# Kernel optimization log

Measured on AMD Instinct MI355X. Metric: run time of the kernel, lower is better.

The kernel has to match this reference:

```python
import jax, jax.numpy as jnp
import numpy as np

DIM = 1024
HEADS = 16
DIM_HEAD = 64
INNER = HEADS * DIM_HEAD  # 1024
EPS = 1e-5


def layer_norm(x, gamma, beta):
    mu = jnp.mean(x, axis=-1, keepdims=True)
    var = jnp.var(x, axis=-1, keepdims=True)
    return (x - mu) * jax.lax.rsqrt(var + EPS) * gamma + beta


def setup_inputs() -> dict:
    key = jax.random.key(0)
    ks = jax.random.split(key, 8)
    b, n, ctx = 2, 2048, 2048
    x = jax.random.normal(ks[0], (b, n, DIM), dtype=jnp.float32)
    context = jax.random.normal(ks[1], (b, ctx, DIM), dtype=jnp.float32)
    context_mask = jnp.ones((b, ctx), dtype=bool)
    # params (torch Linear weights, stored as [in, out] for x @ W)
    g1 = jnp.ones((DIM,), jnp.float32); b1 = jnp.zeros((DIM,), jnp.float32)
    g2 = jnp.ones((DIM,), jnp.float32); b2 = jnp.zeros((DIM,), jnp.float32)
    s = 1.0 / np.sqrt(DIM)
    Wq = jax.random.normal(ks[2], (DIM, INNER), jnp.float32) * s
    Wkv = jax.random.normal(ks[3], (DIM, 2 * INNER), jnp.float32) * s
    Wo = jax.random.normal(ks[4], (INNER, DIM), jnp.float32) * (1.0 / np.sqrt(INNER))
    bo = jnp.zeros((DIM,), jnp.float32)
    return dict(x=x, context=context, context_mask=context_mask,
                g1=g1, b1=b1, g2=g2, b2=b2, Wq=Wq, Wkv=Wkv, Wo=Wo, bo=bo)


def reference(x, context, context_mask, g1, b1, g2, b2, Wq, Wkv, Wo, bo):
    scale = DIM_HEAD ** -0.5
    xn = layer_norm(x, g1, b1)
    cn = layer_norm(context, g2, b2)
    q = xn @ Wq                                  # [b, i, inner]
    kv_x = xn @ Wkv
    kv_c = cn @ Wkv
    k_in, v_in = jnp.split(kv_x, 2, axis=-1)
    k_c, v_c = jnp.split(kv_c, 2, axis=-1)
    k = jnp.concatenate([k_c, k_in], axis=1)     # [b, j, inner]
    v = jnp.concatenate([v_c, v_in], axis=1)

    def split_heads(t):
        b_, n_, _ = t.shape
        return t.reshape(b_, n_, HEADS, DIM_HEAD).transpose(0, 2, 1, 3)

    q, k, v = map(split_heads, (q, k, v))        # [b, h, n, d]
    q = q * scale
    i, j = q.shape[2], k.shape[2]
    mask_value = -jnp.finfo(q.dtype).max

    sim = jnp.einsum('bhid,bhjd->bhij', q, k)
    # context mask padded with True over the self (input) keys
    cm = jnp.pad(context_mask, ((0, 0), (0, j - context_mask.shape[-1])), constant_values=True)
    sim = jnp.where(cm[:, None, None, :], sim, mask_value)
    # causal mask: key position (shifted) strictly after query position
    causal = jnp.triu(jnp.ones((i, j), dtype=bool), k=j - i + 1)
    sim = jnp.where(causal[None, None], mask_value, sim)

    attn = jax.nn.softmax(sim, axis=-1)
    out = jnp.einsum('bhij,bhjd->bhid', attn, v)
    out = out.transpose(0, 2, 1, 3).reshape(x.shape[0], i, INNER)
    return out @ Wo + bo
```

## Files before the change

kernel.cpp:

```cpp
#include <hip/hip_runtime.h>
#include <hip/hip_bf16.h>

#define BB 2
#define NQ 2048
#define NCTX 2048
#define DIMM 1024
#define NH 16
#define DH 64
#define NKV 4096
#define LOG2E 1.44269504088896340736f

typedef float f32x4  __attribute__((ext_vector_type(4)));
typedef float f32x16 __attribute__((ext_vector_type(16)));
typedef short s16x8  __attribute__((ext_vector_type(8)));
typedef unsigned u32x4 __attribute__((ext_vector_type(4)));

__device__ __forceinline__ unsigned short f2bf(float f){
  __hip_bfloat16 h = __float2bfloat16(f);
  return *reinterpret_cast<unsigned short*>(&h);
}

__device__ __forceinline__ unsigned pk2(float a, float b){
  unsigned r;
  asm("v_cvt_pk_bf16_f32 %0, %1, %2" : "=v"(r) : "v"(a), "v"(b));
  return r;
}

__device__ __forceinline__ void cp16(const void* g, void* l){
  __builtin_amdgcn_global_load_lds(
    (const __attribute__((address_space(1))) unsigned int*)(unsigned long long)g,
    (__attribute__((address_space(3))) unsigned int*)(unsigned int)(unsigned long long)l,
    16, 0, 0);
}

__device__ __forceinline__ f32x16 zero16(){
  f32x16 z;
  #pragma unroll
  for (int i=0;i<16;i++) z[i]=0.f;
  return z;
}

__global__ __launch_bounds__(256) void ln2_kernel(const float* __restrict__ x,
    const float* __restrict__ ctx,
    const float* __restrict__ g1, const float* __restrict__ b1,
    const float* __restrict__ g2, const float* __restrict__ b2,
    unsigned short* __restrict__ xn, unsigned short* __restrict__ cn){
  int row = blockIdx.x;
  const float *src, *g, *bta; unsigned short* dst; int r;
  if (row < BB*NQ){ src = x;   g = g1; bta = b1; dst = xn; r = row; }
  else            { src = ctx; g = g2; bta = b2; dst = cn; r = row - BB*NQ; }
  int t = threadIdx.x;
  const float4* xr = (const float4*)(src + (size_t)r*DIMM);
  float4 v = xr[t];
  float s  = v.x+v.y+v.z+v.w;
  float sq = v.x*v.x+v.y*v.y+v.z*v.z+v.w*v.w;
  #pragma unroll
  for (int off=32; off>0; off>>=1){ s += __shfl_down(s, off); sq += __shfl_down(sq, off); }
  __shared__ float red[8];
  int w = t>>6;
  if ((t&63)==0){ red[w]=s; red[w+4]=sq; }
  __syncthreads();
  s  = red[0]+red[1]+red[2]+red[3];
  sq = red[4]+red[5]+red[6]+red[7];
  float mean = s*(1.0f/DIMM);
  float var  = sq*(1.0f/DIMM) - mean*mean;
  float rstd = rsqrtf(var + 1e-5f);
  float4 gv = ((const float4*)g)[t];
  float4 bv = ((const float4*)bta)[t];
  unsigned int o0 = f2bf((v.x-mean)*rstd*gv.x + bv.x);
  unsigned int o1 = f2bf((v.y-mean)*rstd*gv.y + bv.y);
  unsigned int o2 = f2bf((v.z-mean)*rstd*gv.z + bv.z);
  unsigned int o3 = f2bf((v.w-mean)*rstd*gv.w + bv.w);
  uint2 pk; pk.x = o0 | (o1<<16); pk.y = o2 | (o3<<16);
  ((uint2*)(dst + (size_t)r*DIMM))[t] = pk;
}

__global__ __launch_bounds__(256) void wconv3_kernel(const float* __restrict__ Wq,
    const float* __restrict__ Wkv, const float* __restrict__ Wo,
    unsigned short* __restrict__ wpk, unsigned short* __restrict__ woT){
  __shared__ float tile[32][33];
  int bx = blockIdx.x;
  const float* src; unsigned short* dst; int N; float scale; int nb;
  if (bx < 32)      { src=Wq;  dst=wpk;                      N=1024; scale=0.125f; nb=bx; }
  else if (bx < 96) { src=Wkv; dst=wpk + (size_t)1024*1024;  N=2048; scale=1.0f;   nb=bx-32; }
  else              { src=Wo;  dst=woT;                      N=1024; scale=1.0f;   nb=bx-96; }
  int n0 = nb*32, k0 = blockIdx.y*32;
  int c = threadIdx.x & 31, r0 = threadIdx.x >> 5;
  #pragma unroll
  for (int i=0;i<4;i++){
    int r = r0 + i*8;
    tile[r][c] = src[(size_t)(k0+r)*N + n0 + c];
  }
  __syncthreads();
  #pragma unroll
  for (int i=0;i<4;i++){
    int r = r0 + i*8;
    dst[(size_t)(n0+r)*1024 + k0 + c] = f2bf(tile[c][r]*scale);
  }
}

#define BM 128
#define BN 128
#define BK 64
template<int MODE>
__global__ __launch_bounds__(256) void gemm_kernel(
    const unsigned short* __restrict__ A,
    const unsigned short* __restrict__ BT,
    unsigned short* __restrict__ D0,
    unsigned short* __restrict__ D1,
    unsigned short* __restrict__ D2,
    float* __restrict__ FO,
    const float* __restrict__ bias,
    int K){
  __shared__ unsigned short As[BM*BK];
  __shared__ unsigned short Bs[BN*BK];
  int t = threadIdx.x;
  int w = t>>6, l = t&63, lr = l&15, lg = l>>4;
  int wm = w>>1, wn = w&1;
  const unsigned short* Ab = A  + (size_t)(blockIdx.y*BM)*K;
  const unsigned short* Bb = BT + (size_t)(blockIdx.x*BN)*K;
  f32x4 acc[4][4];
  #pragma unroll
  for (int i=0;i<4;i++)
    #pragma unroll
    for (int j=0;j<4;j++) acc[i][j] = (f32x4){0.f,0.f,0.f,0.f};
  int nk = K >> 6;
  for (int kt=0; kt<nk; ++kt){
    __syncthreads();
    #pragma unroll
    for (int q=0;q<4;q++){
      int row = w*32 + q*8 + (l>>3);
      size_t go = (size_t)row*K + kt*64 + (l&7)*8;
      cp16(Ab + go, &As[(w*32+q*8)*64]);
      cp16(Bb + go, &Bs[(w*32+q*8)*64]);
    }
    __syncthreads();
    #pragma unroll
    for (int kk=0;kk<2;kk++){
      s16x8 af[4], bfr[4];
      #pragma unroll
      for (int mf=0;mf<4;mf++) af[mf]  = *(const s16x8*)&As[(wm*64+mf*16+lr)*64 + kk*32 + lg*8];
      #pragma unroll
      for (int nf=0;nf<4;nf++) bfr[nf] = *(const s16x8*)&Bs[(wn*64+nf*16+lr)*64 + kk*32 + lg*8];
      #pragma unroll
      for (int mf=0;mf<4;mf++)
        #pragma unroll
        for (int nf=0;nf<4;nf++)
          acc[mf][nf] = __builtin_amdgcn_mfma_f32_16x16x32_bf16(af[mf], bfr[nf], acc[mf][nf], 0,0,0);
    }
  }
  int rbase = blockIdx.y*BM + wm*64;
  int cbase = blockIdx.x*BN + wn*64;
  #pragma unroll
  for (int mf=0;mf<4;mf++){
    #pragma unroll
    for (int nf=0;nf<4;nf++){
      #pragma unroll
      for (int rr=0;rr<4;rr++){
        int r = rbase + mf*16 + lg*4 + rr;
        int c = cbase + nf*16 + lr;
        float val = acc[mf][nf][rr];
        if (MODE == 2){
          FO[(size_t)r*1024 + c] = val + bias[c];
        } else if (MODE == 0){
          int b = r >> 11, rl = r & 2047;
          unsigned short bv = f2bf(val);
          if (c < 1024)      D0[((size_t)b*NQ + rl)*1024 + c] = bv;
          else if (c < 2048) D1[((size_t)b*NKV + NCTX + rl)*1024 + (c-1024)] = bv;
          else               D2[((size_t)b*NKV + NCTX + rl)*1024 + (c-2048)] = bv;
        } else {
          int b = r >> 11, rl = r & 2047;
          unsigned short bv = f2bf(val);
          if (c < 1024) D0[((size_t)b*NKV + rl)*1024 + c] = bv;
          else          D1[((size_t)b*NKV + rl)*1024 + (c-1024)] = bv;
        }
      }
    }
  }
}

__global__ __launch_bounds__(256) void vtrans_kernel(const unsigned short* __restrict__ V,
    unsigned short* __restrict__ VT){
  __shared__ unsigned short tl[64][72];
  int j0 = blockIdx.x*64, h = blockIdx.y, b = blockIdx.z;
  int tid = threadIdx.x;
  int r = tid>>3, c8 = (tid&7)*8;
  const unsigned short* src = V + ((size_t)(b*NKV + j0))*1024 + h*64;
  #pragma unroll
  for (int p=0;p<2;p++){
    int row = r + p*32;
    *(s16x8*)&tl[row][c8] = *(const s16x8*)(src + (size_t)row*1024 + c8);
  }
  __syncthreads();
  unsigned short* dst = VT + ((size_t)(b*16+h)*64)*4096 + j0;
  #pragma unroll
  for (int p=0;p<2;p++){
    int d = r + p*32;
    s16x8 o;
    #pragma unroll
    for (int e=0;e<8;e++) o[e] = (short)tl[c8+e][d];
    *(s16x8*)(dst + (size_t)d*4096 + c8) = o;
  }
}

__global__ __launch_bounds__(256) void attn_kernel(
    const unsigned short* __restrict__ Q,
    const unsigned short* __restrict__ Kg,
    const unsigned short* __restrict__ VT,
    unsigned short* __restrict__ O){
  __shared__ unsigned short Ks[64*64];
  __shared__ unsigned short Vs[64*64];
  int bx = blockIdx.x;
  int qb = 15 - (bx >> 5);
  int hb = bx & 31;
  int h = hb & 15, b = hb >> 4;
  int i0 = qb*128;
  int tid = threadIdx.x;
  int w = tid>>6, l = tid&63;
  int q5 = l&31, hi = l>>5;

  int row0 = tid>>3, sl = tid&7;
  const unsigned short* Kb = Kg + (size_t)b*NKV*1024 + h*64;
  const unsigned short* Vb = VT + ((size_t)(b*16+h)*64)*4096;
  size_t kg0 = (size_t)row0*1024 + sl*8;
  size_t kg1 = kg0 + (size_t)32*1024;
  size_t vg0 = (size_t)row0*4096 + sl*8;
  size_t vg1 = vg0 + (size_t)32*4096;
  int sw0 = row0*128      + ((sl*16) ^ ((row0&7)<<4));
  int sw1 = (row0+32)*128 + ((sl*16) ^ ((row0&7)<<4));

  const unsigned short* Qr = Q + ((size_t)(b*NQ + i0 + w*32 + q5))*1024 + h*64 + hi*8;
  s16x8 qf[4];
  #pragma unroll
  for (int t=0;t<4;t++) qf[t] = *(const s16x8*)(Qr + t*16);

  f32x16 o0 = zero16(), o1 = zero16();
  float mref = -1e30f, m2 = 0.f, lsum = 0.f;

  int nkb = (NCTX + i0 + 128) >> 6;
  s16x8 kr0 = *(const s16x8*)(Kb + kg0);
  s16x8 kr1 = *(const s16x8*)(Kb + kg1);
  s16x8 vr0 = *(const s16x8*)(Vb + vg0);
  s16x8 vr1 = *(const s16x8*)(Vb + vg1);

  for (int kb=0; kb<nkb; ++kb){
    int j0 = kb*64;
    __syncthreads();
    *(s16x8*)((char*)Ks + sw0) = kr0;
    *(s16x8*)((char*)Ks + sw1) = kr1;
    *(s16x8*)((char*)Vs + sw0) = vr0;
    *(s16x8*)((char*)Vs + sw1) = vr1;
    if (kb+1 < nkb){
      size_t ko = (size_t)(kb+1)*64*1024;
      int vo = (kb+1)*64;
      kr0 = *(const s16x8*)(Kb + ko + kg0);
      kr1 = *(const s16x8*)(Kb + ko + kg1);
      vr0 = *(const s16x8*)(Vb + vo + vg0);
      vr1 = *(const s16x8*)(Vb + vo + vg1);
    }
    __syncthreads();

    f32x16 s0 = zero16(), s1 = zero16();
    __builtin_amdgcn_s_setprio(1);
    #pragma unroll
    for (int t=0;t<4;t++){
      int xo = (t*32 + hi*16) ^ ((q5&7)<<4);
      s16x8 kf0 = *(const s16x8*)((char*)Ks + q5*128 + xo);
      s16x8 kf1 = *(const s16x8*)((char*)Ks + (q5+32)*128 + xo);
      s0 = __builtin_amdgcn_mfma_f32_32x32x16_bf16(kf0, qf[t], s0, 0,0,0);
      s1 = __builtin_amdgcn_mfma_f32_32x32x16_bf16(kf1, qf[t], s1, 0,0,0);
    }
    __builtin_amdgcn_s_setprio(0);

    if (j0 + 63 > NCTX + i0 + w*32){
      int iq = i0 + w*32 + q5;
      #pragma unroll
      for (int r=0;r<16;r++){
        int j = j0 + ((r&3)+8*(r>>2)+4*hi);
        if (j      > NCTX + iq) s0[r] = -1e30f;
        if (j + 32 > NCTX + iq) s1[r] = -1e30f;
      }
    }

    float t0=-1e30f, t1=-1e30f, t2=-1e30f, t3=-1e30f;
    #pragma unroll
    for (int r=0;r<16;r+=4){
      t0 = fmaxf(t0, fmaxf(s0[r  ], s1[r  ]));
      t1 = fmaxf(t1, fmaxf(s0[r+1], s1[r+1]));
      t2 = fmaxf(t2, fmaxf(s0[r+2], s1[r+2]));
      t3 = fmaxf(t3, fmaxf(s0[r+3], s1[r+3]));
    }
    float pm = fmaxf(fmaxf(t0,t1), fmaxf(t2,t3));
    pm = fmaxf(pm, __shfl_xor(pm, 32));
    if (__any(pm - mref > 8.0f)){
      float mnew = fmaxf(mref, pm);
      float alpha = exp2f((mref - mnew)*LOG2E);
      mref = mnew; m2 = mnew*LOG2E;
      lsum *= alpha;
      int ai = __builtin_bit_cast(int, alpha);
      #pragma unroll
      for (int r=0;r<16;r++){
        int cr = (r&3)+8*(r>>2)+4*hi;
        float av = __builtin_bit_cast(float, __builtin_amdgcn_ds_bpermute(cr<<2, ai));
        o0[r] *= av; o1[r] *= av;
      }
    }
    float e0=0.f, e1=0.f, e2=0.f, e3=0.f;
    #pragma unroll
    for (int r=0;r<16;r+=4){
      float a0 = exp2f(fmaf(s0[r  ], LOG2E, -m2));
      float a1 = exp2f(fmaf(s0[r+1], LOG2E, -m2));
      float a2 = exp2f(fmaf(s0[r+2], LOG2E, -m2));
      float a3 = exp2f(fmaf(s0[r+3], LOG2E, -m2));
      float b0 = exp2f(fmaf(s1[r  ], LOG2E, -m2));
      float b1 = exp2f(fmaf(s1[r+1], LOG2E, -m2));
      float b2 = exp2f(fmaf(s1[r+2], LOG2E, -m2));
      float b3 = exp2f(fmaf(s1[r+3], LOG2E, -m2));
      s0[r]=a0; s0[r+1]=a1; s0[r+2]=a2; s0[r+3]=a3;
      s1[r]=b0; s1[r+1]=b1; s1[r+2]=b2; s1[r+3]=b3;
      e0 += a0 + b0; e1 += a1 + b1; e2 += a2 + b2; e3 += a3 + b3;
    }
    float ps = (e0+e1) + (e2+e3);
    ps += __shfl_xor(ps, 32);
    lsum += ps;

    s16x8 pa[4];
    #pragma unroll
    for (int t=0;t<4;t++){
      const f32x16& pp = (t<2) ? s0 : s1;
      int B8 = (t&1)*8;
      unsigned u0 = pk2(pp[B8+0], pp[B8+1]);
      unsigned u1 = pk2(pp[B8+2], pp[B8+3]);
      unsigned v0 = pk2(pp[B8+4], pp[B8+5]);
      unsigned v1 = pk2(pp[B8+6], pp[B8+7]);
      asm("v_permlane32_swap_b32 %0, %1" : "+v"(u0), "+v"(v0));
      asm("v_permlane32_swap_b32 %0, %1" : "+v"(u1), "+v"(v1));
      pa[t] = __builtin_bit_cast(s16x8, (u32x4){u0, u1, v0, v1});
    }

    __builtin_amdgcn_s_setprio(1);
    #pragma unroll
    for (int t=0;t<4;t++){
      int xo = (t*32 + hi*16) ^ ((q5&7)<<4);
      s16x8 vb0 = *(const s16x8*)((char*)Vs + q5*128 + xo);
      s16x8 vb1 = *(const s16x8*)((char*)Vs + (q5+32)*128 + xo);
      o0 = __builtin_amdgcn_mfma_f32_32x32x16_bf16(pa[t], vb0, o0, 0,0,0);
      o1 = __builtin_amdgcn_mfma_f32_32x32x16_bf16(pa[t], vb1, o1, 0,0,0);
    }
    __builtin_amdgcn_s_setprio(0);
  }

  float inv = 1.0f/lsum;
  int ii = __builtin_bit_cast(int, inv);
  #pragma unroll
  for (int r=0;r<16;r++){
    int cr = (r&3)+8*(r>>2)+4*hi;
    float sc = __builtin_bit_cast(float, __builtin_amdgcn_ds_bpermute(cr<<2, ii));
    int qg = i0 + w*32 + cr;
    unsigned short* op = O + ((size_t)(b*NQ + qg))*1024 + h*64 + q5;
    op[0]  = f2bf(o0[r]*sc);
    op[32] = f2bf(o1[r]*sc);
  }
}

extern "C" void kernel_launch(void* const* d_in, const int* in_sizes, int n_in,
                              void* d_out, int out_size, void* d_ws, size_t ws_size,
                              hipStream_t stream){
  const float* x   = (const float*)d_in[0];
  const float* ctx = (const float*)d_in[1];
  const float* g1  = (const float*)d_in[3];
  const float* b1  = (const float*)d_in[4];
  const float* g2  = (const float*)d_in[5];
  const float* b2  = (const float*)d_in[6];
  const float* Wq  = (const float*)d_in[7];
  const float* Wkv = (const float*)d_in[8];
  const float* Wo  = (const float*)d_in[9];
  const float* bo  = (const float*)d_in[10];
  float* out = (float*)d_out;

  unsigned short* xn  = (unsigned short*)d_ws;
  unsigned short* cn  = xn  + (size_t)BB*NQ*DIMM;
  unsigned short* qbf = cn  + (size_t)BB*NCTX*DIMM;
  unsigned short* kbf = qbf + (size_t)BB*NQ*1024;
  unsigned short* vbf = kbf + (size_t)BB*NKV*1024;
  unsigned short* oa  = vbf + (size_t)BB*NKV*1024;
  unsigned short* wpk = oa  + (size_t)BB*NQ*1024;
  unsigned short* woT = wpk + (size_t)3072*1024;
  unsigned short* vT  = xn;

  wconv3_kernel<<<dim3(128,32),256,0,stream>>>(Wq, Wkv, Wo, wpk, woT);
  ln2_kernel<<<dim3(BB*(NQ+NCTX)),256,0,stream>>>(x, ctx, g1, b1, g2, b2, xn, cn);
  gemm_kernel<0><<<dim3(3072/BN,(BB*NQ)/BM),256,0,stream>>>(
      xn, wpk, qbf, kbf, vbf, nullptr, nullptr, 1024);
  gemm_kernel<1><<<dim3(2048/BN,(BB*NCTX)/BM),256,0,stream>>>(
      cn, wpk + (size_t)1024*1024, kbf, vbf, nullptr, nullptr, nullptr, 1024);
  vtrans_kernel<<<dim3(64,16,2),256,0,stream>>>(vbf, vT);
  attn_kernel<<<dim3(512),256,0,stream>>>(qbf, kbf, vT, oa);
  gemm_kernel<2><<<dim3(1024/BN,(BB*NQ)/BM),256,0,stream>>>(
      oa, woT, nullptr, nullptr, nullptr, out, bo, 1024);
}
```

Baseline: 343.5 us.

## Merge QKV and context KV GEMMs into one pipelined 256x256 tile kernel

Replaces the two separate projection GEMM launches with one 320-block kernel using 256x256 tiles, 512 threads and 8 waves. The kernel streams K slices into LDS through a multi-buffered async copy pipeline with explicit vmcnt waits, barriers and setprio around the MFMA bursts. The aim is more data reuse per tile, memory latency hidden behind compute, and one fewer launch. In exchange it uses 128KB of LDS, limiting occupancy to one block per CU, and only 320 blocks exist to cover the GPU.

```diff
diff --git a/kernel.cpp b/kernel.cpp
--- a/kernel.cpp
+++ b/kernel.cpp
@@ -99,16 +99,132 @@
   }
 }
 
+__global__ __launch_bounds__(512) void qkv8_kernel(
+    const unsigned short* __restrict__ Xn,
+    const unsigned short* __restrict__ Cn,
+    const unsigned short* __restrict__ Wpk,
+    unsigned short* __restrict__ Qb,
+    unsigned short* __restrict__ Kb2,
+    unsigned short* __restrict__ Vb2){
+  __shared__ __align__(16) unsigned short As[4][128*64];
+  __shared__ __align__(16) unsigned short Bsh[4][128*64];
+  int bx = blockIdx.x;
+  const unsigned short *Abase, *Bbase; int mt, nt, isctx;
+  if (bx < 192){ Abase = Xn; Bbase = Wpk; mt = bx/12; nt = bx%12; isctx = 0; }
+  else { int b2 = bx-192; Abase = Cn; Bbase = Wpk + (size_t)1024*1024; mt = b2/8; nt = b2%8; isctx = 1; }
+  const char* Ab = (const char*)(Abase + (size_t)mt*256*1024);
+  const char* Bb = (const char*)(Bbase + (size_t)nt*256*1024);
+  int tid = threadIdx.x; int w = tid>>6, l = tid&63;
+  int wm = w>>2, wn = w&3, lr15 = l&15, lg = l>>4;
+  f32x4 acc[8][4];
+  #pragma unroll
+  for (int i=0;i<8;i++)
+    #pragma unroll
+    for (int j=0;j<4;j++) acc[i][j] = (f32x4){0.f,0.f,0.f,0.f};
+
+#define STAGEA(kt,h,par) do{ \
+  char* _l = (char*)As + ((par)*2+(h))*16384; \
+  _Pragma("unroll") for (int _q=0;_q<2;_q++){ \
+    int _c = tid + _q*512; int _lr = _c>>3; int _kb = (_c&7)*16; \
+    int _gr = ((_lr>>6)*128) + (h)*64 + (_lr&63); \
+    cp16(Ab + (size_t)_gr*2048 + (size_t)(kt)*128 + _kb, _l + _c*16); \
+  } }while(0)
+#define STAGEB(kt,h,par) do{ \
+  char* _l = (char*)Bsh + ((par)*2+(h))*16384; \
+  _Pragma("unroll") for (int _q=0;_q<2;_q++){ \
+    int _c = tid + _q*512; int _lr = _c>>3; int _kb = (_c&7)*16; \
+    int _gr = ((_lr>>5)*64) + (h)*32 + (_lr&31); \
+    cp16(Bb + (size_t)_gr*2048 + (size_t)(kt)*128 + _kb, _l + _c*16); \
+  } }while(0)
+#define VM4 asm volatile("s_waitcnt vmcnt(4)" ::: "memory")
+#define VM0 asm volatile("s_waitcnt vmcnt(0)" ::: "memory")
+#define NOST ((void)0)
+#define PHASE(mh,nh,par,STG,WAITV) do{ \
+  s16x8 _af[4][2], _bf[2][2]; \
+  const char* _pa = (const char*)As + ((par)*2+(mh))*16384; \
+  const char* _pb = (const char*)Bsh + ((par)*2+(nh))*16384; \
+  _Pragma("unroll") for (int _j=0;_j<4;_j++) \
+    _Pragma("unroll") for (int _kk=0;_kk<2;_kk++) \
+      _af[_j][_kk] = *(const s16x8*)(_pa + (wm*64 + _j*16 + lr15)*128 + _kk*64 + lg*16); \
+  _Pragma("unroll") for (int _jn=0;_jn<2;_jn++) \
+    _Pragma("unroll") for (int _kk=0;_kk<2;_kk++) \
+      _bf[_jn][_kk] = *(const s16x8*)(_pb + (wn*32 + _jn*16 + lr15)*128 + _kk*64 + lg*16); \
+  STG; \
+  WAITV; \
+  __builtin_amdgcn_s_barrier(); \
+  asm volatile("s_waitcnt lgkmcnt(0)" ::: "memory"); \
+  __builtin_amdgcn_sched_barrier(0); \
+  __builtin_amdgcn_s_setprio(1); \
+  _Pragma("unroll") for (int _j=0;_j<4;_j++) \
+    _Pragma("unroll") for (int _jn=0;_jn<2;_jn++){ \
+      acc[(mh)*4+_j][(nh)*2+_jn] = __builtin_amdgcn_mfma_f32_16x16x32_bf16(_af[_j][0], _bf[_jn][0], acc[(mh)*4+_j][(nh)*2+_jn], 0,0,0); \
+      acc[(mh)*4+_j][(nh)*2+_jn] = __builtin_amdgcn_mfma_f32_16x16x32_bf16(_af[_j][1], _bf[_jn][1], acc[(mh)*4+_j][(nh)*2+_jn], 0,0,0); \
+    } \
+  __builtin_amdgcn_s_setprio(0); \
+  __builtin_amdgcn_s_barrier(); }while(0)
+
+  STAGEA(0,0,0); STAGEB(0,0,0); STAGEA(0,1,0); STAGEB(0,1,0);
+  STAGEA(1,0,1); STAGEB(1,0,1);
+  VM4;
+  __builtin_amdgcn_s_barrier();
+
+  for (int i=0;i<7;i++){
+    int c = 2*i;
+    PHASE(0,0,0, STAGEA(c+1,1,1), NOST);
+    PHASE(0,1,0, STAGEB(c+1,1,1), NOST);
+    PHASE(1,0,0, STAGEA(c+2,0,0), NOST);
+    PHASE(1,1,0, STAGEB(c+2,0,0), VM4);
+    PHASE(0,0,1, STAGEA(c+2,1,0), NOST);
+    PHASE(0,1,1, STAGEB(c+2,1,0), NOST);
+    PHASE(1,0,1, STAGEA(c+3,0,1), NOST);
+    PHASE(1,1,1, STAGEB(c+3,0,1), VM4);
+  }
+  PHASE(0,0,0, STAGEA(15,1,1), NOST);
+  PHASE(0,1,0, STAGEB(15,1,1), NOST);
+  PHASE(1,0,0, NOST, NOST);
+  PHASE(1,1,0, NOST, VM0);
+  PHASE(0,0,1, NOST, NOST);
+  PHASE(0,1,1, NOST, NOST);
+  PHASE(1,0,1, NOST, NOST);
+  PHASE(1,1,1, NOST, NOST);
+
+  int nblk = nt>>2;
+  int coff = (nt&3)*256 + wn*64;
+  #pragma unroll
+  for (int fq=0; fq<8; fq++){
+    #pragma unroll
+    for (int fn=0; fn<4; fn++){
+      #pragma unroll
+      for (int rr=0; rr<4; rr++){
+        int r = mt*256 + wm*128 + fq*16 + lg*4 + rr;
+        int cc = coff + fn*16 + lr15;
+        int b = r>>11, rl = r&2047;
+        unsigned short bv = f2bf(acc[fq][fn][rr]);
+        if (!isctx){
+          if (nblk==0)      Qb [((size_t)b*NQ  + rl)*1024 + cc] = bv;
+          else if (nblk==1) Kb2[((size_t)b*NKV + NCTX + rl)*1024 + cc] = bv;
+          else              Vb2[((size_t)b*NKV + NCTX + rl)*1024 + cc] = bv;
+        } else {
+          if (nblk==0)      Kb2[((size_t)b*NKV + rl)*1024 + cc] = bv;
+          else              Vb2[((size_t)b*NKV + rl)*1024 + cc] = bv;
+        }
+      }
+    }
+  }
+#undef STAGEA
+#undef STAGEB
+#undef VM4
+#undef VM0
+#undef NOST
+#undef PHASE
+}
+
 #define BM 128
 #define BN 128
 #define BK 64
-template<int MODE>
-__global__ __launch_bounds__(256) void gemm_kernel(
+__global__ __launch_bounds__(256) void gemm2_kernel(
     const unsigned short* __restrict__ A,
     const unsigned short* __restrict__ BT,
-    unsigned short* __restrict__ D0,
-    unsigned short* __restrict__ D1,
-    unsigned short* __restrict__ D2,
     float* __restrict__ FO,
     const float* __restrict__ bias,
     int K){
@@ -159,21 +275,7 @@
       for (int rr=0;rr<4;rr++){
         int r = rbase + mf*16 + lg*4 + rr;
         int c = cbase + nf*16 + lr;
-        float val = acc[mf][nf][rr];
-        if (MODE == 2){
-          FO[(size_t)r*1024 + c] = val + bias[c];
-        } else if (MODE == 0){
-          int b = r >> 11, rl = r & 2047;
-          unsigned short bv = f2bf(val);
-          if (c < 1024)      D0[((size_t)b*NQ + rl)*1024 + c] = bv;
-          else if (c < 2048) D1[((size_t)b*NKV + NCTX + rl)*1024 + (c-1024)] = bv;
-          else               D2[((size_t)b*NKV + NCTX + rl)*1024 + (c-2048)] = bv;
-        } else {
-          int b = r >> 11, rl = r & 2047;
-          unsigned short bv = f2bf(val);
-          if (c < 1024) D0[((size_t)b*NKV + rl)*1024 + c] = bv;
-          else          D1[((size_t)b*NKV + rl)*1024 + (c-1024)] = bv;
-        }
+        FO[(size_t)r*1024 + c] = acc[mf][nf][rr] + bias[c];
       }
     }
   }
@@ -390,12 +492,9 @@
 
   wconv3_kernel<<<dim3(128,32),256,0,stream>>>(Wq, Wkv, Wo, wpk, woT);
   ln2_kernel<<<dim3(BB*(NQ+NCTX)),256,0,stream>>>(x, ctx, g1, b1, g2, b2, xn, cn);
-  gemm_kernel<0><<<dim3(3072/BN,(BB*NQ)/BM),256,0,stream>>>(
-      xn, wpk, qbf, kbf, vbf, nullptr, nullptr, 1024);
-  gemm_kernel<1><<<dim3(2048/BN,(BB*NCTX)/BM),256,0,stream>>>(
-      cn, wpk + (size_t)1024*1024, kbf, vbf, nullptr, nullptr, nullptr, 1024);
+  qkv8_kernel<<<dim3(320),512,0,stream>>>(xn, cn, wpk, qbf, kbf, vbf);
   vtrans_kernel<<<dim3(64,16,2),256,0,stream>>>(vbf, vT);
   attn_kernel<<<dim3(512),256,0,stream>>>(qbf, kbf, vT, oa);
-  gemm_kernel<2><<<dim3(1024/BN,(BB*NQ)/BM),256,0,stream>>>(
-      oa, woT, nullptr, nullptr, nullptr, out, bo, 1024);
-}
+  gemm2_kernel<<<dim3(1024/BN,(BB*NQ)/BM),256,0,stream>>>(
+      oa, woT, out, bo, 1024);
+}
```

New measurement: 383.2 us. 1.12x slower.
